# Optimization experiments

Measured on AMD Instinct MI355X. Metric: run time of the kernel, lower is better.

Reference implementation:

```python
import jax, jax.numpy as jnp
import numpy as np

B, S, D = 2, 2048, 2560
H, HD = 32, 80           # n_head, head_dim = n_embd // n_head
RD = 32                  # rotary_dim (partial rotary, phi-style)
ROPE_BASE = 10000.0


def _rope_cache(seqlen, rotary_dim):
    # inv_freq = 1 / base^(2i/d); freqs = outer(t, inv_freq)  -> [S, RD//2]
    inv_freq = 1.0 / (ROPE_BASE ** (jnp.arange(0, rotary_dim, 2, dtype=jnp.float32) / rotary_dim))
    t = jnp.arange(seqlen, dtype=jnp.float32)
    freqs = jnp.outer(t, inv_freq)
    return jnp.cos(freqs), jnp.sin(freqs)


def setup_inputs() -> dict:
    key = jax.random.key(0)
    k0, k1, k2, k3, k4 = jax.random.split(key, 5)
    x = jax.random.normal(k0, (B, S, D), dtype=jnp.float32)
    wqkv_w = jax.random.normal(k1, (3 * D, D), dtype=jnp.float32) * 0.02
    wqkv_b = jax.random.normal(k2, (3 * D,), dtype=jnp.float32) * 0.02
    out_w = jax.random.normal(k3, (D, D), dtype=jnp.float32) * 0.02
    out_b = jax.random.normal(k4, (D,), dtype=jnp.float32) * 0.02
    return {"x": x, "wqkv_w": wqkv_w, "wqkv_b": wqkv_b, "out_w": out_w, "out_b": out_b}


def _attention_core(x, wqkv_w, wqkv_b, out_w, out_b):
    b, s, d = x.shape
    qkv = (x @ wqkv_w.T + wqkv_b).reshape(b, s, 3, H, HD)  # [B,S,3,H,HD]

    cos, sin = _rope_cache(s, RD)            # [S, RD//2]
    c = cos[:, None, :]                       # [S,1,RD//2]
    si = sin[:, None, :]

    def rot(t):  # partial NeoX-style rotary on first RD dims; t: [B,S,H,HD]
        t_rot, t_pass = t[..., :RD], t[..., RD:]
        t1, t2 = t_rot[..., : RD // 2], t_rot[..., RD // 2 :]
        return jnp.concatenate([t1 * c - t2 * si, t1 * si + t2 * c, t_pass], axis=-1)

    q = rot(qkv[:, :, 0])                     # [B,S,H,HD]
    k = rot(qkv[:, :, 1])
    v = qkv[:, :, 2]

    # fp32 scores = q @ (k * scale)^T, causal mask filled with -10000.0 (as in source)
    scale = 1.0 / np.sqrt(HD).astype(np.float32)
    scores = jnp.einsum("bqhd,bkhd->bhqk", q, k * scale)  # [B,H,S,S]
    causal_mask = jnp.arange(s)[None, :] > jnp.arange(s)[:, None]  # cols > rows
    scores = jnp.where(causal_mask, jnp.float32(-10000.0), scores)
    attn = jax.nn.softmax(scores, axis=-1)
    ctx = jnp.einsum("bhqk,bkhd->bqhd", attn, v).reshape(b, s, d)
    return ctx @ out_w.T + out_b


def reference(x, wqkv_w, wqkv_b, out_w, out_b):
    return _attention_core(x, wqkv_w, wqkv_b, out_w, out_b)
```

## Files before the change

kernel.cpp:

```cpp
#include <hip/hip_runtime.h>
#include <cstdint>
#include <cstddef>

#define B_  2
#define S_  2048
#define D_  2560
#define H_  32
#define HD_ 80

typedef __attribute__((ext_vector_type(8))) short  short8;
typedef __attribute__((ext_vector_type(4))) float  floatx4;

__device__ __forceinline__ float b2f(unsigned short u) {
  union { unsigned int i; float f; } x; x.i = ((unsigned int)u) << 16; return x.f;
}
__device__ __forceinline__ unsigned short f2bf(float f) {
  union { float f; unsigned int i; } x; x.f = f;
  unsigned int u = x.i;
  return (unsigned short)((u + 0x7fffu + ((u >> 16) & 1u)) >> 16);
}

__global__ void cvt3_kernel(const float* __restrict__ s0, unsigned short* __restrict__ d0, int n0,
                            const float* __restrict__ s1, unsigned short* __restrict__ d1, int n1,
                            const float* __restrict__ s2, unsigned short* __restrict__ d2, int n2) {
  int j = blockIdx.x * 256 + threadIdx.x;
  const float* s; unsigned short* d;
  if (j < n0) { s = s0; d = d0; }
  else {
    j -= n0;
    if (j < n1) { s = s1; d = d1; }
    else { j -= n1; if (j >= n2) return; s = s2; d = d2; }
  }
  const float4 v = ((const float4*)s)[j];
  ushort4 r;
  r.x = f2bf(v.x); r.y = f2bf(v.y); r.z = f2bf(v.z); r.w = f2bf(v.w);
  ((ushort4*)d)[j] = r;
}

#define GLOAD_LDS16(g, l)                                                      \
  __builtin_amdgcn_global_load_lds(                                            \
      (const __attribute__((address_space(1))) void*)(g),                      \
      (__attribute__((address_space(3))) void*)(l), 16, 0, 0)

template <int OUT_BF16>
__global__ __launch_bounds__(256)
void gemm_bt(const unsigned short* __restrict__ A,
             const unsigned short* __restrict__ B,
             const float* __restrict__ bias,
             void* __restrict__ Cv,
             const int M, const int N, const int K) {
  __shared__ unsigned short As[128 * 32];
  __shared__ unsigned short Bs[128 * 32];
  const int tid  = threadIdx.x;
  const int wave = tid >> 6;
  const int lane = tid & 63;
  const int wm   = (wave & 1) << 6;
  const int wn   = (wave >> 1) << 6;
  const int row0 = (int)blockIdx.y << 7;
  const int col0 = (int)blockIdx.x << 7;
  const unsigned short* Ab = A + (size_t)row0 * K;
  const unsigned short* Bb = B + (size_t)col0 * K;
  const int srow = wave * 16 + (lane >> 2);
  const int scol = (lane & 3) << 3;
  const int fr = lane & 15;
  const int fq = (lane >> 4) << 3;
  floatx4 acc[4][4] = {};

  for (int k0 = 0; k0 < K; k0 += 32) {
    __syncthreads();
    GLOAD_LDS16(Ab + (size_t)srow        * K + (k0 + scol), &As[wave * 512]);
    GLOAD_LDS16(Ab + (size_t)(srow + 64) * K + (k0 + scol), &As[2048 + wave * 512]);
    GLOAD_LDS16(Bb + (size_t)srow        * K + (k0 + scol), &Bs[wave * 512]);
    GLOAD_LDS16(Bb + (size_t)(srow + 64) * K + (k0 + scol), &Bs[2048 + wave * 512]);
    __syncthreads();
    short8 aF[4], bF[4];
#pragma unroll
    for (int i = 0; i < 4; i++) aF[i] = *(const short8*)(&As[(wm + i * 16 + fr) * 32 + fq]);
#pragma unroll
    for (int i = 0; i < 4; i++) bF[i] = *(const short8*)(&Bs[(wn + i * 16 + fr) * 32 + fq]);
#pragma unroll
    for (int mi = 0; mi < 4; mi++)
#pragma unroll
      for (int ni = 0; ni < 4; ni++)
        acc[mi][ni] = __builtin_amdgcn_mfma_f32_16x16x32_bf16(aF[mi], bF[ni], acc[mi][ni], 0, 0, 0);
  }

  const int cr = (lane >> 4) << 2;
  const int cn = lane & 15;
  unsigned short* Cb = (unsigned short*)Cv;
  float* Cf = (float*)Cv;
#pragma unroll
  for (int ni = 0; ni < 4; ni++) {
    const int col = col0 + wn + ni * 16 + cn;
    const float bv = bias[col];
#pragma unroll
    for (int mi = 0; mi < 4; mi++) {
      const int rowb = row0 + wm + mi * 16 + cr;
#pragma unroll
      for (int r = 0; r < 4; r++) {
        const float v = acc[mi][ni][r] + bv;
        const size_t idx = (size_t)(rowb + r) * N + col;
        if (OUT_BF16) Cb[idx] = f2bf(v);
        else          Cf[idx] = v;
      }
    }
  }
}

__global__ void rope_kernel(const unsigned short* __restrict__ qkv,
                            unsigned short* __restrict__ Q,
                            unsigned short* __restrict__ K) {
  const int idx = blockIdx.x * 256 + threadIdx.x;
  if (idx >= B_ * S_ * H_) return;
  const int h = idx & (H_ - 1);
  const int s = (idx >> 5) & (S_ - 1);
  const int b = idx >> 16;
  const unsigned short* row = qkv + (size_t)(b * S_ + s) * (3 * D_);
  const size_t obase = ((size_t)(b * H_ + h) * S_ + s) * HD_;

  float cc[16], ssn[16];
#pragma unroll
  for (int i = 0; i < 16; i++) {
    const float ang = (float)s * exp2f((float)i * -0.83048202372184059f);
    ssn[i] = sinf(ang);
    cc[i]  = cosf(ang);
  }
  {
    const float QS = 0.11180339887498949f * 1.4426950408889634f;
    const uint4* src = (const uint4*)(row + h * HD_);
    float f[80], g[80];
#pragma unroll
    for (int i = 0; i < 10; i++) {
      uint4 t = src[i];
      const unsigned short* w = (const unsigned short*)&t;
#pragma unroll
      for (int j = 0; j < 8; j++) f[i * 8 + j] = b2f(w[j]);
    }
#pragma unroll
    for (int i = 0; i < 16; i++) {
      g[i]      = f[i] * cc[i] - f[i + 16] * ssn[i];
      g[i + 16] = f[i] * ssn[i] + f[i + 16] * cc[i];
    }
#pragma unroll
    for (int i = 32; i < 80; i++) g[i] = f[i];
    uint4* dst = (uint4*)(Q + obase);
#pragma unroll
    for (int i = 0; i < 10; i++) {
      uint4 t;
      unsigned short* w = (unsigned short*)&t;
#pragma unroll
      for (int j = 0; j < 8; j++) w[j] = f2bf(g[i * 8 + j] * QS);
      dst[i] = t;
    }
  }
  {
    const uint4* src = (const uint4*)(row + (H_ + h) * HD_);
    float f[32], g[32];
#pragma unroll
    for (int i = 0; i < 4; i++) {
      uint4 t = src[i];
      const unsigned short* w = (const unsigned short*)&t;
#pragma unroll
      for (int j = 0; j < 8; j++) f[i * 8 + j] = b2f(w[j]);
    }
#pragma unroll
    for (int i = 0; i < 16; i++) {
      g[i]      = f[i] * cc[i] - f[i + 16] * ssn[i];
      g[i + 16] = f[i] * ssn[i] + f[i + 16] * cc[i];
    }
    uint4* dst = (uint4*)(K + obase);
#pragma unroll
    for (int i = 0; i < 4; i++) {
      uint4 t;
      unsigned short* w = (unsigned short*)&t;
#pragma unroll
      for (int j = 0; j < 8; j++) w[j] = f2bf(g[i * 8 + j]);
      dst[i] = t;
    }
#pragma unroll
    for (int i = 4; i < 10; i++) dst[i] = src[i];
  }
}

__global__ __launch_bounds__(256)
void vtrans_kernel(const unsigned short* __restrict__ qkv, unsigned short* __restrict__ Vt) {
  __shared__ unsigned short T[64][88];
  const int tid = threadIdx.x;
  const int bh = blockIdx.y;
  const int b = bh >> 5, h = bh & 31;
  const int tile = blockIdx.x;
  const int s0 = tile * 64;
  for (int t = tid; t < 640; t += 256) {
    const int r = t / 10, c = t % 10;
    const size_t src = ((size_t)((b * S_ + s0 + r) * 3) + 2) * D_ + h * HD_ + c * 8;
    *(uint4*)&T[r][c * 8] = *(const uint4*)&qkv[src];
  }
  __syncthreads();
  unsigned short* tb = Vt + ((size_t)bh * 32 + tile) * 5120;
  for (int t = tid; t < 640; t += 256) {
    const int d = t / 8, sc = t % 8;
    uint4 o;
    unsigned short* w = (unsigned short*)&o;
#pragma unroll
    for (int j = 0; j < 8; j++) w[j] = T[sc * 8 + j][d];
    *(uint4*)&tb[d * 64 + ((sc * 8) ^ ((d & 7) * 8))] = o;
  }
}

__global__ __launch_bounds__(256, 4)
void attn_mfma(const unsigned short* __restrict__ Qg,
               const unsigned short* __restrict__ Kg,
               const unsigned short* __restrict__ Vtg,
               unsigned short* __restrict__ ctx) {
  __shared__ unsigned short Ks[64 * 80];
  __shared__ unsigned short Vs[80 * 64];
  __shared__ unsigned short Ts[4][32 * 40];

  const int tid  = threadIdx.x;
  const int wave = tid >> 6;
  const int lane = tid & 63;
  const int fr   = lane & 15;
  const int fg   = lane >> 4;
  const int bh   = blockIdx.y;
  const int qt   = (int)gridDim.x - 1 - (int)blockIdx.x;
  const int qbase = (qt << 7) + wave * 32;

  const unsigned short* Qrow  = Qg  + (size_t)bh * S_ * HD_;
  const unsigned short* Krow  = Kg  + (size_t)bh * S_ * HD_;
  const unsigned short* Vtile = Vtg + (size_t)bh * 32 * 5120;

  short8 qf[2][3];
  const short8 zfrag = {};
#pragma unroll
  for (int mi = 0; mi < 2; mi++) {
    const unsigned short* qp = Qrow + (size_t)(qbase + mi * 16 + fr) * HD_;
    qf[mi][0] = *(const short8*)&qp[fg * 8];
    qf[mi][1] = *(const short8*)&qp[32 + fg * 8];
    qf[mi][2] = (fg < 2) ? *(const short8*)&qp[64 + fg * 8] : zfrag;
  }

  floatx4 accOT[5][2] = {};
  float l_part[2] = {0.f, 0.f};

  const int nch = 2 * qt + 2;
  for (int c = 0; c < nch; c++) {
    const int k0 = c * 64;
    __syncthreads();
    {
      const unsigned short* Kt = Krow + (size_t)k0 * HD_;
      for (int i = wave; i < 10; i += 4)
        GLOAD_LDS16(Kt + i * 512 + lane * 8, &Ks[i * 512]);
    }
    {
      const unsigned short* Vt = Vtile + (size_t)c * 5120;
      for (int i = wave; i < 10; i += 4)
        GLOAD_LDS16(Vt + i * 512 + lane * 8, &Vs[i * 512]);
    }
    __syncthreads();

    floatx4 accST[4][2] = {};
#pragma unroll
    for (int ni = 0; ni < 4; ni++) {
      const unsigned short* kp = &Ks[(ni * 16 + fr) * 80];
      const short8 kf0 = *(const short8*)&kp[fg * 8];
      const short8 kf1 = *(const short8*)&kp[32 + fg * 8];
      const short8 kf2 = *(const short8*)&kp[64 + (fg & 1) * 8];
      accST[ni][0] = __builtin_amdgcn_mfma_f32_16x16x32_bf16(kf0, qf[0][0], accST[ni][0], 0, 0, 0);
      accST[ni][1] = __builtin_amdgcn_mfma_f32_16x16x32_bf16(kf0, qf[1][0], accST[ni][1], 0, 0, 0);
      accST[ni][0] = __builtin_amdgcn_mfma_f32_16x16x32_bf16(kf1, qf[0][1], accST[ni][0], 0, 0, 0);
      accST[ni][1] = __builtin_amdgcn_mfma_f32_16x16x32_bf16(kf1, qf[1][1], accST[ni][1], 0, 0, 0);
      accST[ni][0] = __builtin_amdgcn_mfma_f32_16x16x32_bf16(kf2, qf[0][2], accST[ni][0], 0, 0, 0);
      accST[ni][1] = __builtin_amdgcn_mfma_f32_16x16x32_bf16(kf2, qf[1][2], accST[ni][1], 0, 0, 0);
    }

    if (k0 + 63 > qbase) {
#pragma unroll
      for (int ni = 0; ni < 4; ni++)
#pragma unroll
        for (int mi = 0; mi < 2; mi++) {
          const int qg = qbase + mi * 16 + fr;
#pragma unroll
          for (int r = 0; r < 4; r++) {
            const int kg = k0 + ni * 16 + fg * 4 + r;
            if (kg > qg) accST[ni][mi][r] = -1e30f;
          }
        }
    }

#pragma unroll
    for (int hh = 0; hh < 2; hh++) {
#pragma unroll
      for (int nh = 0; nh < 2; nh++) {
        const int ni = hh * 2 + nh;
#pragma unroll
        for (int mi = 0; mi < 2; mi++) {
          const float p0 = __builtin_amdgcn_exp2f(accST[ni][mi][0]);
          const float p1 = __builtin_amdgcn_exp2f(accST[ni][mi][1]);
          const float p2 = __builtin_amdgcn_exp2f(accST[ni][mi][2]);
          const float p3 = __builtin_amdgcn_exp2f(accST[ni][mi][3]);
          l_part[mi] += (p0 + p1) + (p2 + p3);
          uint2 w;
          w.x = (unsigned)f2bf(p0) | ((unsigned)f2bf(p1) << 16);
          w.y = (unsigned)f2bf(p2) | ((unsigned)f2bf(p3) << 16);
          *(uint2*)&Ts[wave][(mi * 16 + fr) * 40 + nh * 16 + fg * 4] = w;
        }
      }
      const short8 pf0 = *(const short8*)&Ts[wave][fr * 40 + fg * 8];
      const short8 pf1 = *(const short8*)&Ts[wave][(16 + fr) * 40 + fg * 8];
      const int vcol = hh * 32 + fg * 8;
#pragma unroll
      for (int dt = 0; dt < 5; dt++) {
        const short8 vf = *(const short8*)&Vs[(dt * 16 + fr) * 64 + (vcol ^ ((fr & 7) * 8))];
        accOT[dt][0] = __builtin_amdgcn_mfma_f32_16x16x32_bf16(vf, pf0, accOT[dt][0], 0, 0, 0);
        accOT[dt][1] = __builtin_amdgcn_mfma_f32_16x16x32_bf16(vf, pf1, accOT[dt][1], 0, 0, 0);
      }
    }
  }

  const int b = bh >> 5, h2 = bh & 31;
#pragma unroll
  for (int mi = 0; mi < 2; mi++) {
    float s = l_part[mi];
    s += __shfl_xor(s, 16);
    s += __shfl_xor(s, 32);
    const float inv = 1.f / s;
    const size_t rowoff = (size_t)(b * S_ + qbase + mi * 16 + fr) * D_ + h2 * HD_;
#pragma unroll
    for (int dt = 0; dt < 5; dt++) {
      const float v0 = accOT[dt][mi][0] * inv;
      const float v1 = accOT[dt][mi][1] * inv;
      const float v2 = accOT[dt][mi][2] * inv;
      const float v3 = accOT[dt][mi][3] * inv;
      uint2 w;
      w.x = (unsigned)f2bf(v0) | ((unsigned)f2bf(v1) << 16);
      w.y = (unsigned)f2bf(v2) | ((unsigned)f2bf(v3) << 16);
      *(uint2*)&ctx[rowoff + dt * 16 + fg * 4] = w;
    }
  }
}

extern "C" void kernel_launch(void* const* d_in, const int* in_sizes, int n_in,
                              void* d_out, int out_size, void* d_ws, size_t ws_size,
                              hipStream_t stream) {
  (void)in_sizes; (void)n_in; (void)out_size; (void)ws_size;
  const float* x      = (const float*)d_in[0];
  const float* wqkv_w = (const float*)d_in[1];
  const float* wqkv_b = (const float*)d_in[2];
  const float* out_w  = (const float*)d_in[3];
  const float* out_b  = (const float*)d_in[4];
  char* ws = (char*)d_ws;

  unsigned short* Xb    = (unsigned short*)(ws + 0);
  unsigned short* Wqkvb = (unsigned short*)(ws + 20971520);
  unsigned short* qkv   = (unsigned short*)(ws + 60293120);
  unsigned short* Qb    = (unsigned short*)(ws + 123207680);
  unsigned short* Kb    = (unsigned short*)(ws + 144179200);
  unsigned short* Woutb = (unsigned short*)(ws + 165150720);
  unsigned short* ctx   = Xb;
  unsigned short* Vtile = (unsigned short*)(ws + 34078720);

  cvt3_kernel<<<35840, 256, 0, stream>>>(x, Xb, 2621440,
                                         wqkv_w, Wqkvb, 4915200,
                                         out_w, Woutb, 1638400);
  gemm_bt<1><<<dim3(60, 32), 256, 0, stream>>>(Xb, Wqkvb, wqkv_b, (void*)qkv, 4096, 7680, 2560);
  rope_kernel<<<512, 256, 0, stream>>>(qkv, Qb, Kb);
  vtrans_kernel<<<dim3(32, 64), 256, 0, stream>>>(qkv, Vtile);
  attn_mfma<<<dim3(16, 64), 256, 0, stream>>>(Qb, Kb, Vtile, ctx);
  gemm_bt<0><<<dim3(20, 32), 256, 0, stream>>>(ctx, Woutb, out_b, d_out, 4096, 2560, 2560);
}
```

Baseline: 652.3 us.

## Replace GEMM with 256x256 double-buffered, swizzled-LDS, 8-wave pipelined kernel

Replaces the 128x128 single-buffered bf16 GEMM with a 256x256-tile, 512-thread kernel. It double-buffers 64-wide K slices in 128KB of LDS and uses an XOR-swizzled layout to avoid bank conflicts. Global-to-LDS loads for the next tiles are interleaved with MFMA phases using explicit waitcnt, barriers and setprio. This cuts global traffic per FLOP and hides load latency. The trade-offs are larger tiles that leave fewer blocks (160 for the output projection, below the CU count), higher register pressure, and fragile hand-tuned synchronization.

```diff
diff --git a/kernel.cpp b/kernel.cpp
--- a/kernel.cpp
+++ b/kernel.cpp
@@ -43,62 +43,164 @@
       (__attribute__((address_space(3))) void*)(l), 16, 0, 0)
 
 template <int OUT_BF16>
-__global__ __launch_bounds__(256)
-void gemm_bt(const unsigned short* __restrict__ A,
-             const unsigned short* __restrict__ B,
+__global__ __launch_bounds__(512)
+void gemm256(const unsigned short* __restrict__ A,
+             const unsigned short* __restrict__ Bw,
              const float* __restrict__ bias,
              void* __restrict__ Cv,
              const int M, const int N, const int K) {
-  __shared__ unsigned short As[128 * 32];
-  __shared__ unsigned short Bs[128 * 32];
+  __shared__ __align__(16) unsigned short sh[65536];
   const int tid  = threadIdx.x;
   const int wave = tid >> 6;
   const int lane = tid & 63;
-  const int wm   = (wave & 1) << 6;
-  const int wn   = (wave >> 1) << 6;
-  const int row0 = (int)blockIdx.y << 7;
-  const int col0 = (int)blockIdx.x << 7;
-  const unsigned short* Ab = A + (size_t)row0 * K;
-  const unsigned short* Bb = B + (size_t)col0 * K;
-  const int srow = wave * 16 + (lane >> 2);
-  const int scol = (lane & 3) << 3;
+  const int wm = wave >> 2;
+  const int wn = wave & 3;
   const int fr = lane & 15;
-  const int fq = (lane >> 4) << 3;
-  floatx4 acc[4][4] = {};
-
-  for (int k0 = 0; k0 < K; k0 += 32) {
-    __syncthreads();
-    GLOAD_LDS16(Ab + (size_t)srow        * K + (k0 + scol), &As[wave * 512]);
-    GLOAD_LDS16(Ab + (size_t)(srow + 64) * K + (k0 + scol), &As[2048 + wave * 512]);
-    GLOAD_LDS16(Bb + (size_t)srow        * K + (k0 + scol), &Bs[wave * 512]);
-    GLOAD_LDS16(Bb + (size_t)(srow + 64) * K + (k0 + scol), &Bs[2048 + wave * 512]);
-    __syncthreads();
-    short8 aF[4], bF[4];
-#pragma unroll
-    for (int i = 0; i < 4; i++) aF[i] = *(const short8*)(&As[(wm + i * 16 + fr) * 32 + fq]);
-#pragma unroll
-    for (int i = 0; i < 4; i++) bF[i] = *(const short8*)(&Bs[(wn + i * 16 + fr) * 32 + fq]);
-#pragma unroll
-    for (int mi = 0; mi < 4; mi++)
-#pragma unroll
-      for (int ni = 0; ni < 4; ni++)
-        acc[mi][ni] = __builtin_amdgcn_mfma_f32_16x16x32_bf16(aF[mi], bF[ni], acc[mi][ni], 0, 0, 0);
-  }
-
-  const int cr = (lane >> 4) << 2;
-  const int cn = lane & 15;
+  const int fg = lane >> 4;
+  const int row0 = (int)blockIdx.y << 8;
+  const int col0 = (int)blockIdx.x << 8;
+  const unsigned short* Ab = A  + (size_t)row0 * K;
+  const unsigned short* Bb = Bw + (size_t)col0 * K;
+  const int srow = lane >> 2;
+  const int scol = ((lane & 3) << 3) ^ ((lane & 32) ? 16 : 0);
+  const int rdoff = fr * 32 + ((fg * 8) ^ ((fr & 8) ? 16 : 0));
+  const int aOff = wm * 8192;
+  const int bOff = 16384 + (wn >> 1) * 8192;
+  const int rbB  = (wn & 1) * 4;
+  const int NT = K >> 6;
+
+  floatx4 acc[8][4] = {};
+
+#define STAGE_HALF(G, matOff, c, h, k0)                                        \
+  do {                                                                         \
+    _Pragma("unroll")                                                          \
+    for (int i_ = 0; i_ < 2; ++i_) {                                           \
+      const int s_ = (wave << 1) | i_;                                         \
+      const int kk_ = s_ >> 3, rb_ = s_ & 7;                                   \
+      GLOAD_LDS16((G) + (size_t)((h) * 128 + rb_ * 16 + srow) * K              \
+                      + ((k0) + kk_ * 32 + scol),                              \
+                  &sh[(c) * 32768 + (matOff) + (h) * 8192 + s_ * 512]);        \
+    }                                                                          \
+  } while (0)
+
+  STAGE_HALF(Ab, 0,     0, 0, 0);
+  STAGE_HALF(Ab, 0,     0, 1, 0);
+  STAGE_HALF(Bb, 16384, 0, 0, 0);
+  STAGE_HALF(Bb, 16384, 0, 1, 0);
+  if (NT > 1) { STAGE_HALF(Ab, 0, 1, 0, 64); STAGE_HALF(Ab, 0, 1, 1, 64); }
+  if (NT > 1) asm volatile("s_waitcnt vmcnt(4)" ::: "memory");
+  else        asm volatile("s_waitcnt vmcnt(0)" ::: "memory");
+  __builtin_amdgcn_s_barrier();
+
+  for (int t = 0; t < NT; ++t) {
+    const int c  = t & 1;
+    const int cb = c << 15;
+    short8 aF[4][2], bF[2][2];
+#pragma unroll
+    for (int mi = 0; mi < 4; ++mi)
+#pragma unroll
+      for (int kk = 0; kk < 2; ++kk)
+        aF[mi][kk] = *(const short8*)&sh[cb + aOff + (kk * 8 + mi) * 512 + rdoff];
+#pragma unroll
+    for (int nj = 0; nj < 2; ++nj)
+#pragma unroll
+      for (int kk = 0; kk < 2; ++kk)
+        bF[nj][kk] = *(const short8*)&sh[cb + bOff + (kk * 8 + rbB + nj) * 512 + rdoff];
+    if (t + 1 < NT) STAGE_HALF(Bb, 16384, c ^ 1, 0, (t + 1) << 6);
+    __builtin_amdgcn_s_barrier();
+    asm volatile("s_waitcnt lgkmcnt(0)" ::: "memory");
+    __builtin_amdgcn_sched_barrier(0);
+    __builtin_amdgcn_s_setprio(1);
+#pragma unroll
+    for (int kk = 0; kk < 2; ++kk)
+#pragma unroll
+      for (int mi = 0; mi < 4; ++mi)
+#pragma unroll
+        for (int nj = 0; nj < 2; ++nj)
+          acc[mi][nj] = __builtin_amdgcn_mfma_f32_16x16x32_bf16(aF[mi][kk], bF[nj][kk], acc[mi][nj], 0, 0, 0);
+    __builtin_amdgcn_s_setprio(0);
+    __builtin_amdgcn_s_barrier();
+#pragma unroll
+    for (int nj = 0; nj < 2; ++nj)
+#pragma unroll
+      for (int kk = 0; kk < 2; ++kk)
+        bF[nj][kk] = *(const short8*)&sh[cb + bOff + (kk * 8 + rbB + 2 + nj) * 512 + rdoff];
+    if (t + 1 < NT) STAGE_HALF(Bb, 16384, c ^ 1, 1, (t + 1) << 6);
+    __builtin_amdgcn_s_barrier();
+    asm volatile("s_waitcnt lgkmcnt(0)" ::: "memory");
+    __builtin_amdgcn_sched_barrier(0);
+    __builtin_amdgcn_s_setprio(1);
+#pragma unroll
+    for (int kk = 0; kk < 2; ++kk)
+#pragma unroll
+      for (int mi = 0; mi < 4; ++mi)
+#pragma unroll
+        for (int nj = 0; nj < 2; ++nj)
+          acc[mi][2 + nj] = __builtin_amdgcn_mfma_f32_16x16x32_bf16(aF[mi][kk], bF[nj][kk], acc[mi][2 + nj], 0, 0, 0);
+    __builtin_amdgcn_s_setprio(0);
+    __builtin_amdgcn_s_barrier();
+#pragma unroll
+    for (int mi = 0; mi < 4; ++mi)
+#pragma unroll
+      for (int kk = 0; kk < 2; ++kk)
+        aF[mi][kk] = *(const short8*)&sh[cb + aOff + (kk * 8 + 4 + mi) * 512 + rdoff];
+#pragma unroll
+    for (int nj = 0; nj < 2; ++nj)
+#pragma unroll
+      for (int kk = 0; kk < 2; ++kk)
+        bF[nj][kk] = *(const short8*)&sh[cb + bOff + (kk * 8 + rbB + nj) * 512 + rdoff];
+    __builtin_amdgcn_s_barrier();
+    asm volatile("s_waitcnt lgkmcnt(0)" ::: "memory");
+    __builtin_amdgcn_sched_barrier(0);
+    __builtin_amdgcn_s_setprio(1);
+#pragma unroll
+    for (int kk = 0; kk < 2; ++kk)
+#pragma unroll
+      for (int mi = 0; mi < 4; ++mi)
+#pragma unroll
+        for (int nj = 0; nj < 2; ++nj)
+          acc[4 + mi][nj] = __builtin_amdgcn_mfma_f32_16x16x32_bf16(aF[mi][kk], bF[nj][kk], acc[4 + mi][nj], 0, 0, 0);
+    __builtin_amdgcn_s_setprio(0);
+    __builtin_amdgcn_s_barrier();
+#pragma unroll
+    for (int nj = 0; nj < 2; ++nj)
+#pragma unroll
+      for (int kk = 0; kk < 2; ++kk)
+        bF[nj][kk] = *(const short8*)&sh[cb + bOff + (kk * 8 + rbB + 2 + nj) * 512 + rdoff];
+    if (t + 2 < NT) {
+      STAGE_HALF(Ab, 0, c, 0, (t + 2) << 6);
+      STAGE_HALF(Ab, 0, c, 1, (t + 2) << 6);
+    }
+    __builtin_amdgcn_s_barrier();
+    asm volatile("s_waitcnt lgkmcnt(0)" ::: "memory");
+    __builtin_amdgcn_sched_barrier(0);
+    __builtin_amdgcn_s_setprio(1);
+#pragma unroll
+    for (int kk = 0; kk < 2; ++kk)
+#pragma unroll
+      for (int mi = 0; mi < 4; ++mi)
+#pragma unroll
+        for (int nj = 0; nj < 2; ++nj)
+          acc[4 + mi][2 + nj] = __builtin_amdgcn_mfma_f32_16x16x32_bf16(aF[mi][kk], bF[nj][kk], acc[4 + mi][2 + nj], 0, 0, 0);
+    __builtin_amdgcn_s_setprio(0);
+    if (t + 2 < NT)      asm volatile("s_waitcnt vmcnt(4)" ::: "memory");
+    else if (t + 1 < NT) asm volatile("s_waitcnt vmcnt(0)" ::: "memory");
+    __builtin_amdgcn_s_barrier();
+  }
+#undef STAGE_HALF
+
   unsigned short* Cb = (unsigned short*)Cv;
   float* Cf = (float*)Cv;
 #pragma unroll
-  for (int ni = 0; ni < 4; ni++) {
-    const int col = col0 + wn + ni * 16 + cn;
+  for (int nj = 0; nj < 4; ++nj) {
+    const int col = col0 + wn * 64 + nj * 16 + fr;
     const float bv = bias[col];
 #pragma unroll
-    for (int mi = 0; mi < 4; mi++) {
-      const int rowb = row0 + wm + mi * 16 + cr;
-#pragma unroll
-      for (int r = 0; r < 4; r++) {
-        const float v = acc[mi][ni][r] + bv;
+    for (int mi = 0; mi < 8; ++mi) {
+      const int rowb = row0 + wm * 128 + mi * 16 + fg * 4;
+#pragma unroll
+      for (int r = 0; r < 4; ++r) {
+        const float v = acc[mi][nj][r] + bv;
         const size_t idx = (size_t)(rowb + r) * N + col;
         if (OUT_BF16) Cb[idx] = f2bf(v);
         else          Cf[idx] = v;
@@ -362,9 +464,9 @@
   cvt3_kernel<<<35840, 256, 0, stream>>>(x, Xb, 2621440,
                                          wqkv_w, Wqkvb, 4915200,
                                          out_w, Woutb, 1638400);
-  gemm_bt<1><<<dim3(60, 32), 256, 0, stream>>>(Xb, Wqkvb, wqkv_b, (void*)qkv, 4096, 7680, 2560);
+  gemm256<1><<<dim3(30, 16), 512, 0, stream>>>(Xb, Wqkvb, wqkv_b, (void*)qkv, 4096, 7680, 2560);
   rope_kernel<<<512, 256, 0, stream>>>(qkv, Qb, Kb);
   vtrans_kernel<<<dim3(32, 64), 256, 0, stream>>>(qkv, Vtile);
   attn_mfma<<<dim3(16, 64), 256, 0, stream>>>(Qb, Kb, Vtile, ctx);
-  gemm_bt<0><<<dim3(20, 32), 256, 0, stream>>>(ctx, Woutb, out_b, d_out, 4096, 2560, 2560);
-}
+  gemm256<0><<<dim3(10, 16), 512, 0, stream>>>(ctx, Woutb, out_b, d_out, 4096, 2560, 2560);
+}
```

Measured after the change: 604.1 us. 7.4% less time.
